# Kernel tuning notes

Hardware: AMD Instinct MI355X
Metric: run time of the kernel (lower is better)

Reference implementation:

```python
import jax, jax.numpy as jnp
import numpy as np

TAU = 0.07
HARD_RATIO = 0.3
N_T = 8192
N_S = 8192
F_DIM = 128
P_DIM = 128
BN_EPS = 1e-5
GRID_B, GRID_Z, GRID_Y, GRID_X = 2, 64, 128, 128


def _project(x, w1, b1, w2, b2, gamma, beta):
    # Linear -> ReLU -> Linear -> BatchNorm1d (training-mode batch stats) -> L2 normalize
    h = jax.nn.relu(x @ w1 + b1)
    h = h @ w2 + b2
    mu = h.mean(axis=0)
    var = h.var(axis=0)  # biased, matching torch BN normalization
    h = (h - mu) * jax.lax.rsqrt(var + BN_EPS) * gamma + beta
    return h / jnp.linalg.norm(h, axis=1, keepdims=True)


def _coord_key(c):
    # unique int key per (b,z,y,x) cell; fits easily in int32 for this grid
    return ((c[:, 0] * GRID_Z + c[:, 1]) * GRID_Y + c[:, 2]) * GRID_X + c[:, 3]


def setup_inputs() -> dict:
    rng = np.random.default_rng(0)
    total = GRID_B * GRID_Z * GRID_Y * GRID_X
    perm = rng.permutation(total)
    t_lin = perm[:N_T]  # unique teacher voxel cells
    n_overlap = N_S // 2  # half the student voxels coincide with teacher voxels
    s_lin = np.concatenate([t_lin[:n_overlap], perm[N_T:N_T + (N_S - n_overlap)]])
    s_lin = rng.permutation(s_lin)

    def lin2coord(l):
        x = l % GRID_X; l = l // GRID_X
        y = l % GRID_Y; l = l // GRID_Y
        z = l % GRID_Z; b = l // GRID_Z
        return np.stack([b, z, y, x], axis=1).astype(np.int32)

    key = jax.random.key(0)
    ks = jax.random.split(key, 8)

    def lin_w(k, fan_in, fan_out):
        return jax.random.normal(k, (fan_in, fan_out), jnp.float32) / np.float32(np.sqrt(fan_in))

    return {
        'teacher_features': jax.random.normal(ks[0], (N_T, F_DIM), jnp.float32),
        'student_features': jax.random.normal(ks[1], (N_S, F_DIM), jnp.float32),
        't_w1': lin_w(ks[2], F_DIM, F_DIM), 't_b1': jnp.zeros((F_DIM,), jnp.float32),
        't_w2': lin_w(ks[3], F_DIM, P_DIM), 't_b2': jnp.zeros((P_DIM,), jnp.float32),
        't_gamma': jnp.ones((P_DIM,), jnp.float32), 't_beta': jnp.zeros((P_DIM,), jnp.float32),
        's_w1': lin_w(ks[4], F_DIM, F_DIM), 's_b1': jnp.zeros((F_DIM,), jnp.float32),
        's_w2': lin_w(ks[5], F_DIM, P_DIM), 's_b2': jnp.zeros((P_DIM,), jnp.float32),
        's_gamma': jnp.ones((P_DIM,), jnp.float32), 's_beta': jnp.zeros((P_DIM,), jnp.float32),
        'teacher_coords': jnp.asarray(lin2coord(t_lin)),
        'student_coords': jnp.asarray(lin2coord(s_lin)),
    }


def reference(teacher_features, student_features,
              t_w1, t_b1, t_w2, t_b2, t_gamma, t_beta,
              s_w1, s_b1, s_w2, s_b2, s_gamma, s_beta,
              teacher_coords, student_coords):
    t_proj = _project(teacher_features, t_w1, t_b1, t_w2, t_b2, t_gamma, t_beta)  # [N_t, P]
    s_proj = _project(student_features, s_w1, s_b1, s_w2, s_b2, s_gamma, s_beta)  # [N_s, P]

    # hash-based positive matching (teacher coords are unique cells)
    tk = _coord_key(teacher_coords)  # [N_t]
    sk = _coord_key(student_coords)  # [N_s]
    eq = sk[:, None] == tk[None, :]  # [N_s, N_t] bool
    matched = eq.any(axis=1)         # [N_s]
    t_idx = jnp.argmax(eq, axis=1)   # matching teacher index (garbage where unmatched, masked below)

    pos_sim = jnp.sum(s_proj * t_proj[t_idx], axis=1) / TAU  # [N_s]
    neg_sim = (s_proj @ t_proj.T) / TAU                       # [N_s, N_t] full teacher pool

    # hard negative mining: top-k most similar negatives per student
    k = max(1, int(N_T * HARD_RATIO))
    hard_neg, _ = jax.lax.top_k(neg_sim, k)                   # [N_s, k]

    all_sims = jnp.concatenate([pos_sim[:, None], hard_neg], axis=1)  # [N_s, 1+k]
    per_pair = -jax.nn.log_softmax(all_sims, axis=1)[:, 0]

    m = matched.astype(per_pair.dtype)
    loss = jnp.sum(per_pair * m) / jnp.maximum(jnp.sum(m), 1.0)
    return loss
```

## Files before the change

kernel.cpp:

```cpp
#include <hip/hip_runtime.h>
#include <hip/hip_bf16.h>

#define NT 8192
#define NS 8192
#define FD 128
#define PD 128
#define KTOP 2457
#define TAUINV 14.285714285714286f
#define NBIN 512
#define HSIZE 65536
#define HMASK 65535
#define CAND_MAX 1024
#define NMC 4096

typedef __attribute__((ext_vector_type(8))) short s16x8;
typedef __attribute__((ext_vector_type(4))) float f32x4;

__device__ __forceinline__ float bf2f(unsigned short u) {
  return __uint_as_float(((unsigned)u) << 16);
}
__device__ __forceinline__ unsigned short f2bf(float x) {
  unsigned u = __float_as_uint(x);
  return (unsigned short)((u + 0x7FFF + ((u >> 16) & 1)) >> 16);
}

__global__ __launch_bounds__(256) void init_ws(float* stats, int* hkey, int* nmatch)
{
  int i = blockIdx.x * 256 + threadIdx.x;
  if (i < 512) stats[i] = 0.f;
  if (i < HSIZE) hkey[i] = -1;
  if (i == 0) *nmatch = 0;
}

__global__ __launch_bounds__(256) void proj_mlp2(
    const float* __restrict__ Xt, const float* __restrict__ Xs2,
    const float* __restrict__ tW1, const float* __restrict__ tB1,
    const float* __restrict__ tW2, const float* __restrict__ tB2,
    const float* __restrict__ sW1, const float* __restrict__ sB1,
    const float* __restrict__ sW2, const float* __restrict__ sB2,
    float* __restrict__ Ht, float* __restrict__ Hs2, float* __restrict__ stats)
{
  int f = blockIdx.y;
  const float* X  = f ? Xs2 : Xt;
  const float* W1 = f ? sW1 : tW1;
  const float* B1 = f ? sB1 : tB1;
  const float* W2 = f ? sW2 : tW2;
  const float* B2 = f ? sB2 : tB2;
  float* H        = f ? Hs2 : Ht;
  float* colsum   = stats + f * 256;
  float* colsq    = colsum + 128;

  __shared__ __align__(16) float Xs[32][128];
  __shared__ __align__(16) float H1s[32][128];
  __shared__ float cs[128], cq[128];
  int tid = threadIdx.x;
  int r0 = blockIdx.x * 32;
  for (int i = tid; i < 32 * 32; i += 256) {
    int r = i >> 5, q = i & 31;
    ((float4*)Xs[r])[q] = ((const float4*)(X + (size_t)(r0 + r) * FD))[q];
  }
  if (tid < 128) { cs[tid] = 0.f; cq[tid] = 0.f; }
  __syncthreads();

  int c  = (tid & 63) * 2;
  int rg = (tid >> 6) * 8;
  float a0[8], a1[8];
  #pragma unroll
  for (int r = 0; r < 8; ++r) { a0[r] = 0.f; a1[r] = 0.f; }
  for (int k = 0; k < FD; ++k) {
    float2 w = *(const float2*)(W1 + k * FD + c);
    #pragma unroll
    for (int r = 0; r < 8; ++r) {
      float x = Xs[rg + r][k];
      a0[r] = fmaf(x, w.x, a0[r]);
      a1[r] = fmaf(x, w.y, a1[r]);
    }
  }
  float2 b = *(const float2*)(B1 + c);
  #pragma unroll
  for (int r = 0; r < 8; ++r) {
    H1s[rg + r][c]     = fmaxf(a0[r] + b.x, 0.f);
    H1s[rg + r][c + 1] = fmaxf(a1[r] + b.y, 0.f);
  }
  __syncthreads();

  #pragma unroll
  for (int r = 0; r < 8; ++r) { a0[r] = 0.f; a1[r] = 0.f; }
  for (int k = 0; k < FD; ++k) {
    float2 w = *(const float2*)(W2 + k * PD + c);
    #pragma unroll
    for (int r = 0; r < 8; ++r) {
      float x = H1s[rg + r][k];
      a0[r] = fmaf(x, w.x, a0[r]);
      a1[r] = fmaf(x, w.y, a1[r]);
    }
  }
  b = *(const float2*)(B2 + c);
  float s0 = 0.f, s1 = 0.f, q0 = 0.f, q1 = 0.f;
  #pragma unroll
  for (int r = 0; r < 8; ++r) {
    float h0 = a0[r] + b.x, h1 = a1[r] + b.y;
    *(float2*)(H + (size_t)(r0 + rg + r) * PD + c) = make_float2(h0, h1);
    s0 += h0; s1 += h1; q0 += h0 * h0; q1 += h1 * h1;
  }
  atomicAdd(&cs[c], s0);     atomicAdd(&cs[c + 1], s1);
  atomicAdd(&cq[c], q0);     atomicAdd(&cq[c + 1], q1);
  __syncthreads();
  if (tid < 128) { atomicAdd(&colsum[tid], cs[tid]); atomicAdd(&colsq[tid], cq[tid]); }
}

__global__ __launch_bounds__(256) void bn_l2_2(
    const float* __restrict__ Ht, const float* __restrict__ Hs2,
    const float* __restrict__ stats,
    const float* __restrict__ t_gamma, const float* __restrict__ t_beta,
    const float* __restrict__ s_gamma, const float* __restrict__ s_beta,
    unsigned short* __restrict__ Th, unsigned short* __restrict__ Tl,
    unsigned short* __restrict__ ShC, unsigned short* __restrict__ SlC,
    const int* __restrict__ minv)
{
  int f = blockIdx.y;
  const float* H = f ? Hs2 : Ht;
  const float* colsum = stats + f * 256;
  const float* colsq  = colsum + 128;
  const float* gamma  = f ? s_gamma : t_gamma;
  const float* beta   = f ? s_beta : t_beta;
  unsigned short* Oh  = f ? ShC : Th;
  unsigned short* Ol  = f ? SlC : Tl;
  const float invN = 1.f / (float)NT;

  __shared__ float part[2][2];
  int half = threadIdx.x >> 7;
  int c    = threadIdx.x & 127;
  int wih  = (threadIdx.x >> 6) & 1;
  int row  = blockIdx.x * 2 + half;
  float mu  = colsum[c] * invN;
  float var = colsq[c] * invN - mu * mu;
  float inv = rsqrtf(var + 1e-5f);
  float y = (H[(size_t)row * PD + c] - mu) * inv * gamma[c] + beta[c];
  float sq = y * y;
  #pragma unroll
  for (int off = 32; off >= 1; off >>= 1) sq += __shfl_xor(sq, off, 64);
  if ((threadIdx.x & 63) == 0) part[half][wih] = sq;
  __syncthreads();
  float norm = sqrtf(part[half][0] + part[half][1]);
  float r = y / norm;
  int orow = f ? minv[row] : row;
  if (orow >= 0) {
    unsigned ub = __float_as_uint(r);
    float fhi = __uint_as_float(ub & 0xFFFF0000u);
    float lo  = r - fhi;
    Oh[(size_t)orow * PD + c] = (unsigned short)(ub >> 16);
    Ol[(size_t)orow * PD + c] = (unsigned short)(__float_as_uint(lo) >> 16);
  }
}

__device__ __forceinline__ int coord_key(int4 c) {
  return ((c.x * 64 + c.y) * 128 + c.z) * 128 + c.w;
}

__global__ __launch_bounds__(256) void hash_insert(
    const int* __restrict__ coords, int* __restrict__ hkey, int* __restrict__ hval)
{
  int t = blockIdx.x * 256 + threadIdx.x;
  if (t >= NT) return;
  int key = coord_key(((const int4*)coords)[t]);
  unsigned slot = (((unsigned)key * 2654435761u) >> 16) & HMASK;
  while (true) {
    int old = atomicCAS(&hkey[slot], -1, key);
    if (old == -1) { hval[slot] = t; break; }
    slot = (slot + 1) & HMASK;
  }
}

__global__ __launch_bounds__(256) void hash_lookup(
    const int* __restrict__ coords, const int* __restrict__ hkey,
    const int* __restrict__ hval, int* __restrict__ minv,
    int* __restrict__ mt, int* __restrict__ nmatch)
{
  int s = blockIdx.x * 256 + threadIdx.x;
  if (s >= NS) return;
  int key = coord_key(((const int4*)coords)[s]);
  unsigned slot = (((unsigned)key * 2654435761u) >> 16) & HMASK;
  int res = -1;
  while (true) {
    int k = hkey[slot];
    if (k == key) { res = hval[slot]; break; }
    if (k == -1) break;
    slot = (slot + 1) & HMASK;
  }
  int cslot = -1;
  if (res >= 0) { cslot = atomicAdd(nmatch, 1); mt[cslot] = res; }
  minv[s] = cslot;
}

__global__ __launch_bounds__(256) void pos_exact(
    const unsigned short* __restrict__ ShC, const unsigned short* __restrict__ SlC,
    const unsigned short* __restrict__ Th, const unsigned short* __restrict__ Tl,
    const int* __restrict__ mt, const int* __restrict__ nmatch,
    float* __restrict__ posb)
{
  int lane = threadIdx.x & 63, wid = threadIdx.x >> 6;
  int slot = blockIdx.x * 4 + wid;
  if (slot >= *nmatch) return;
  int t = mt[slot];
  const unsigned short* ah = ShC + (size_t)slot * FD;
  const unsigned short* al = SlC + (size_t)slot * FD;
  const unsigned short* bh = Th + (size_t)t * FD;
  const unsigned short* bl = Tl + (size_t)t * FD;
  float sum = 0.f;
  #pragma unroll
  for (int j = 0; j < 2; ++j) {
    int k = lane * 2 + j;
    float av = bf2f(ah[k]) + bf2f(al[k]);
    float bv = bf2f(bh[k]) + bf2f(bl[k]);
    sum = fmaf(av, bv, sum);
  }
  #pragma unroll
  for (int off = 32; off >= 1; off >>= 1) sum += __shfl_xor(sum, off, 64);
  if (lane == 0) posb[slot] = sum * TAUINV;
}

__device__ __forceinline__ void gload16(const void* g, void* l) {
  __builtin_amdgcn_global_load_lds(
      (const __attribute__((address_space(1))) unsigned int*)g,
      (__attribute__((address_space(3))) unsigned int*)l, 16, 0, 0);
}

__global__ __launch_bounds__(256) void gemm_bf16x2(
    const unsigned short* __restrict__ ShC, const unsigned short* __restrict__ SlC,
    const unsigned short* __restrict__ Th, const unsigned short* __restrict__ Tl,
    unsigned short* __restrict__ Pb, const int* __restrict__ nmatch)
{
  int ay = blockIdx.x, bx = blockIdx.y;
  if (ay * 128 >= *nmatch) return;

  __shared__ unsigned short lds[32768];
  int tid = threadIdx.x, lane = tid & 63, wid = tid >> 6;

  const unsigned short* gB[2] = { Th + (size_t)bx * 128 * FD,
                                  Tl + (size_t)bx * 128 * FD };
  #pragma unroll
  for (int comp = 0; comp < 2; ++comp) {
    const char* g = (const char*)gB[comp];
    char* lb = (char*)lds + comp * 32768;
    #pragma unroll
    for (int it = 0; it < 8; ++it) {
      int chunk0 = it * 256 + wid * 64;
      int d = (chunk0 + lane) * 16;
      int src = d ^ (((d >> 8) & 7) << 4);
      gload16(g + src, lb + chunk0 * 16);
    }
  }

  int wr = wid >> 1, wc = wid & 1;
  const unsigned short* gA_h = ShC + (size_t)(ay * 128) * FD;
  const unsigned short* gA_l = SlC + (size_t)(ay * 128) * FD;
  int rA[4];
  #pragma unroll
  for (int m = 0; m < 4; ++m) rA[m] = wr * 64 + m * 16 + (lane & 15);
  int cA0 = (lane >> 4) * 8;

  s16x8 nah[4], nal[4];
  #pragma unroll
  for (int m = 0; m < 4; ++m) {
    nah[m] = *(const s16x8*)(gA_h + (size_t)rA[m] * FD + cA0);
    nal[m] = *(const s16x8*)(gA_l + (size_t)rA[m] * FD + cA0);
  }
  __syncthreads();

  f32x4 acc[4][4] = {};
  #pragma unroll
  for (int kk = 0; kk < 4; ++kk) {
    s16x8 ah[4], al[4];
    #pragma unroll
    for (int m = 0; m < 4; ++m) { ah[m] = nah[m]; al[m] = nal[m]; }
    if (kk < 3) {
      int cA = (kk + 1) * 32 + cA0;
      #pragma unroll
      for (int m = 0; m < 4; ++m) {
        nah[m] = *(const s16x8*)(gA_h + (size_t)rA[m] * FD + cA);
        nal[m] = *(const s16x8*)(gA_l + (size_t)rA[m] * FD + cA);
      }
    }
    int cB = kk * 32 + cA0;
    s16x8 bh[4], bl[4];
    #pragma unroll
    for (int n = 0; n < 4; ++n) {
      int r = wc * 64 + n * 16 + (lane & 15);
      int byt = r * 256 + ((cB * 2) ^ ((r & 7) << 4));
      bh[n] = *(const s16x8*)((const char*)lds + byt);
      bl[n] = *(const s16x8*)((const char*)lds + 32768 + byt);
    }
    #pragma unroll
    for (int m = 0; m < 4; ++m)
      #pragma unroll
      for (int n = 0; n < 4; ++n) {
        acc[m][n] = __builtin_amdgcn_mfma_f32_16x16x32_bf16(ah[m], bh[n], acc[m][n], 0, 0, 0);
        acc[m][n] = __builtin_amdgcn_mfma_f32_16x16x32_bf16(ah[m], bl[n], acc[m][n], 0, 0, 0);
        acc[m][n] = __builtin_amdgcn_mfma_f32_16x16x32_bf16(al[m], bh[n], acc[m][n], 0, 0, 0);
      }
  }

  #pragma unroll
  for (int m = 0; m < 4; ++m)
    #pragma unroll
    for (int n = 0; n < 4; ++n) {
      int pc = bx * 128 + wc * 64 + n * 16 + (lane & 15);
      int pr0 = ay * 128 + wr * 64 + m * 16 + (lane >> 4) * 4;
      #pragma unroll
      for (int reg = 0; reg < 4; ++reg)
        Pb[(size_t)(pr0 + reg) * NT + pc] = f2bf(acc[m][n][reg] * TAUINV);
    }
}

__global__ __launch_bounds__(256) void select_lse(
    const unsigned short* __restrict__ Pb, const float* __restrict__ posb,
    const int* __restrict__ nmatch, float* __restrict__ perrow)
{
  int slot = blockIdx.x;
  if (slot >= *nmatch) return;

  __shared__ unsigned hist4[4 * NBIN];
  __shared__ unsigned cnt[NBIN];
  __shared__ float cand[CAND_MAX];
  __shared__ float red[4];
  __shared__ int redi[4];
  __shared__ float sh_lo[3], sh_scale[3];
  __shared__ int sh_bin[3];
  __shared__ int sh_B, sh_jrem, sh_cntB;
  __shared__ unsigned sh_cc;
  __shared__ float sh_M;
  __shared__ float sh_theta;

  int tid = threadIdx.x, lane = tid & 63, wid = tid >> 6;
  const unsigned short* p = Pb + (size_t)slot * NT;

  float rr[32];
  float mx = -1e30f;
  #pragma unroll
  for (int q = 0; q < 4; ++q) {
    s16x8 v = ((const s16x8*)p)[tid + 256 * q];
    #pragma unroll
    for (int j = 0; j < 8; ++j) {
      float f = bf2f((unsigned short)v[j]);
      rr[q * 8 + j] = f;
      mx = fmaxf(mx, f);
    }
  }
  #pragma unroll
  for (int off = 32; off >= 1; off >>= 1) mx = fmaxf(mx, __shfl_xor(mx, off, 64));
  if (lane == 0) red[wid] = mx;
  __syncthreads();
  if (tid == 0) sh_M = fmaxf(fmaxf(red[0], red[1]), fmaxf(red[2], red[3]));

  int kneed = KTOP;
  float lo = -14.6f, hi = 14.6f;
  int nlev = 0, jrem = 0, cntB = 0;
  for (int level = 0; level < 3; ++level) {
    float scale = (float)NBIN / (hi - lo);
    for (int i = tid; i < 4 * NBIN; i += 256) hist4[i] = 0;
    __syncthreads();
    unsigned* wh = hist4 + wid * NBIN;
    #pragma unroll
    for (int j = 0; j < 32; ++j) {
      float v = rr[j];
      bool act = true;
      for (int l = 0; l < nlev; ++l) {
        int bb = (int)((v - sh_lo[l]) * sh_scale[l]);
        bb = bb < 0 ? 0 : (bb > NBIN - 1 ? NBIN - 1 : bb);
        act = act && (bb == sh_bin[l]);
      }
      if (act) {
        int bb = (int)((v - lo) * scale);
        bb = bb < 0 ? 0 : (bb > NBIN - 1 ? NBIN - 1 : bb);
        atomicAdd(&wh[bb], 1u);
      }
    }
    __syncthreads();
    for (int i = tid; i < NBIN; i += 256)
      cnt[i] = hist4[i] + hist4[NBIN + i] + hist4[2 * NBIN + i] + hist4[3 * NBIN + i];
    __syncthreads();
    for (int off = 1; off < NBIN; off <<= 1) {
      unsigned c0 = (tid + off < NBIN) ? cnt[tid + off] : 0u;
      unsigned c1 = (tid + 256 + off < NBIN) ? cnt[tid + 256 + off] : 0u;
      __syncthreads();
      cnt[tid] += c0;
      cnt[tid + 256] += c1;
      __syncthreads();
    }
    #pragma unroll
    for (int u = 0; u < 2; ++u) {
      int i = tid + u * 256;
      unsigned si = cnt[i];
      unsigned sn = (i < NBIN - 1) ? cnt[i + 1] : 0u;
      if (si >= (unsigned)kneed && sn < (unsigned)kneed) {
        sh_B = i;
        sh_jrem = kneed - (int)sn;
        sh_cntB = (int)(si - sn);
      }
    }
    __syncthreads();
    int B = sh_B; jrem = sh_jrem; cntB = sh_cntB;
    if (tid == 0) { sh_lo[level] = lo; sh_scale[level] = scale; sh_bin[level] = B; }
    nlev = level + 1;
    if (cntB <= CAND_MAX) break;
    float wdt = (hi - lo) * (1.0f / NBIN);
    lo = lo + (float)B * wdt;
    hi = lo + wdt;
    kneed = jrem;
    __syncthreads();
  }

  if (tid == 0) sh_cc = 0;
  __syncthreads();
  #pragma unroll
  for (int j = 0; j < 32; ++j) {
    float v = rr[j];
    bool act = true;
    for (int l = 0; l < nlev; ++l) {
      int bb = (int)((v - sh_lo[l]) * sh_scale[l]);
      bb = bb < 0 ? 0 : (bb > NBIN - 1 ? NBIN - 1 : bb);
      act = act && (bb == sh_bin[l]);
    }
    if (act) {
      unsigned idx = atomicAdd(&sh_cc, 1u);
      if (idx < CAND_MAX) cand[idx] = v;
    }
  }
  __syncthreads();
  int c = (int)sh_cc; if (c > CAND_MAX) c = CAND_MAX;

  float thl = -1e30f;
  for (int i = tid; i < c; i += 256) {
    float v = cand[i];
    int gt = 0, eq = 0;
    for (int m = 0; m < c; ++m) {
      float u = cand[m];
      gt += (u > v) ? 1 : 0;
      eq += (u == v) ? 1 : 0;
    }
    if (gt < jrem && jrem <= gt + eq) thl = v;
  }
  #pragma unroll
  for (int off = 32; off >= 1; off >>= 1) thl = fmaxf(thl, __shfl_xor(thl, off, 64));
  if (lane == 0) red[wid] = thl;
  __syncthreads();
  if (tid == 0) sh_theta = fmaxf(fmaxf(red[0], red[1]), fmaxf(red[2], red[3]));
  __syncthreads();
  float theta = sh_theta;
  float pos = posb[slot];
  float Mp = fmaxf(sh_M, pos);

  float esum = 0.f; int g = 0;
  #pragma unroll
  for (int j = 0; j < 32; ++j) {
    float v = rr[j];
    if (v > theta) { esum += __expf(v - Mp); g++; }
  }
  #pragma unroll
  for (int off = 32; off >= 1; off >>= 1) {
    esum += __shfl_xor(esum, off, 64);
    g    += __shfl_xor(g, off, 64);
  }
  if (lane == 0) { red[wid] = esum; redi[wid] = g; }
  __syncthreads();
  if (tid == 0) {
    float E = red[0] + red[1] + red[2] + red[3];
    int   G = redi[0] + redi[1] + redi[2] + redi[3];
    float S = E + (float)(KTOP - G) * __expf(theta - Mp) + __expf(pos - Mp);
    perrow[slot] = logf(S) + Mp - pos;
  }
}

__global__ __launch_bounds__(256) void finalize(
    const float* __restrict__ perrow, const int* __restrict__ nmatch,
    float* __restrict__ out)
{
  __shared__ float ssum[4];
  int nm = *nmatch;
  float s = 0.f;
  for (int i = threadIdx.x; i < nm; i += 256) s += perrow[i];
  #pragma unroll
  for (int off = 32; off >= 1; off >>= 1) s += __shfl_xor(s, off, 64);
  int lane = threadIdx.x & 63, wid = threadIdx.x >> 6;
  if (lane == 0) ssum[wid] = s;
  __syncthreads();
  if (threadIdx.x == 0) {
    float S = ssum[0] + ssum[1] + ssum[2] + ssum[3];
    out[0] = S / fmaxf((float)nm, 1.f);
  }
}

extern "C" void kernel_launch(void* const* d_in, const int* in_sizes, int n_in,
                              void* d_out, int out_size, void* d_ws, size_t ws_size,
                              hipStream_t stream)
{
  const float* t_feat  = (const float*)d_in[0];
  const float* s_feat  = (const float*)d_in[1];
  const float* t_w1    = (const float*)d_in[2];
  const float* t_b1    = (const float*)d_in[3];
  const float* t_w2    = (const float*)d_in[4];
  const float* t_b2    = (const float*)d_in[5];
  const float* t_gamma = (const float*)d_in[6];
  const float* t_beta  = (const float*)d_in[7];
  const float* s_w1    = (const float*)d_in[8];
  const float* s_b1    = (const float*)d_in[9];
  const float* s_w2    = (const float*)d_in[10];
  const float* s_b2    = (const float*)d_in[11];
  const float* s_gamma = (const float*)d_in[12];
  const float* s_beta  = (const float*)d_in[13];
  const int*   t_coord = (const int*)d_in[14];
  const int*   s_coord = (const int*)d_in[15];

  char* w = (char*)d_ws;
  unsigned short* Th  = (unsigned short*)(w + 0x000000);
  unsigned short* Tl  = (unsigned short*)(w + 0x200000);
  unsigned short* ShC = (unsigned short*)(w + 0x400000);
  unsigned short* SlC = (unsigned short*)(w + 0x600000);
  float* stats  = (float*)(w + 0x800000);
  int*   hkey   = (int*)(w + 0x800800);
  int*   hval   = (int*)(w + 0x840800);
  int*   nmatch = (int*)(w + 0x880800);
  int*   mt     = (int*)(w + 0x880900);
  int*   minv   = (int*)(w + 0x888900);
  float* perrow = (float*)(w + 0x890900);
  float* posb   = (float*)(w + 0x898900);
  float* Ht     = (float*)(w + 0x8B0000);
  float* Hs     = (float*)(w + 0xCB0000);
  unsigned short* Pb = (unsigned short*)(w + 0x8B0000);

  init_ws<<<HSIZE / 256, 256, 0, stream>>>(stats, hkey, nmatch);
  hash_insert<<<NT / 256, 256, 0, stream>>>(t_coord, hkey, hval);
  hash_lookup<<<NS / 256, 256, 0, stream>>>(s_coord, hkey, hval, minv, mt, nmatch);

  {
    dim3 g(NT / 32, 2);
    proj_mlp2<<<g, 256, 0, stream>>>(t_feat, s_feat,
                                     t_w1, t_b1, t_w2, t_b2,
                                     s_w1, s_b1, s_w2, s_b2,
                                     Ht, Hs, stats);
  }
  {
    dim3 g(NT / 2, 2);
    bn_l2_2<<<g, 256, 0, stream>>>(Ht, Hs, stats, t_gamma, t_beta,
                                   s_gamma, s_beta, Th, Tl, ShC, SlC, minv);
  }
  pos_exact<<<NMC / 4, 256, 0, stream>>>(ShC, SlC, Th, Tl, mt, nmatch, posb);

  {
    dim3 g(NMC / 128, NT / 128);
    gemm_bf16x2<<<g, 256, 0, stream>>>(ShC, SlC, Th, Tl, Pb, nmatch);
  }
  select_lse<<<NMC, 256, 0, stream>>>(Pb, posb, nmatch, perrow);
  finalize<<<1, 256, 0, stream>>>(perrow, nmatch, (float*)d_out);
}
```

Before: 255.6 us.

## Use exact 2-pass radix select on bf16 keys and fuse pos/finalize into select

```diff
diff --git a/kernel.cpp b/kernel.cpp
--- a/kernel.cpp
+++ b/kernel.cpp
@@ -7,10 +7,8 @@
 #define PD 128
 #define KTOP 2457
 #define TAUINV 14.285714285714286f
-#define NBIN 512
 #define HSIZE 65536
 #define HMASK 65535
-#define CAND_MAX 1024
 #define NMC 4096
 
 typedef __attribute__((ext_vector_type(8))) short s16x8;
@@ -23,13 +21,22 @@
   unsigned u = __float_as_uint(x);
   return (unsigned short)((u + 0x7FFF + ((u >> 16) & 1)) >> 16);
 }
-
-__global__ __launch_bounds__(256) void init_ws(float* stats, int* hkey, int* nmatch)
+__device__ __forceinline__ unsigned bf2key(unsigned short u) {
+  return (u & 0x8000u) ? (unsigned)(u ^ 0xFFFFu) : (unsigned)(u ^ 0x8000u);
+}
+__device__ __forceinline__ float key2f(unsigned key) {
+  unsigned u = (key & 0x8000u) ? (key ^ 0x8000u) : (key ^ 0xFFFFu);
+  return __uint_as_float((u & 0xFFFFu) << 16);
+}
+
+__global__ __launch_bounds__(256) void init_ws(float* stats, int* hkey,
+                                               int* nmatch, float* dsum,
+                                               unsigned* dcnt)
 {
   int i = blockIdx.x * 256 + threadIdx.x;
   if (i < 512) stats[i] = 0.f;
   if (i < HSIZE) hkey[i] = -1;
-  if (i == 0) *nmatch = 0;
+  if (i == 0) { *nmatch = 0; *dsum = 0.f; *dcnt = 0u; }
 }
 
 __global__ __launch_bounds__(256) void proj_mlp2(
@@ -193,33 +200,6 @@
   minv[s] = cslot;
 }
 
-__global__ __launch_bounds__(256) void pos_exact(
-    const unsigned short* __restrict__ ShC, const unsigned short* __restrict__ SlC,
-    const unsigned short* __restrict__ Th, const unsigned short* __restrict__ Tl,
-    const int* __restrict__ mt, const int* __restrict__ nmatch,
-    float* __restrict__ posb)
-{
-  int lane = threadIdx.x & 63, wid = threadIdx.x >> 6;
-  int slot = blockIdx.x * 4 + wid;
-  if (slot >= *nmatch) return;
-  int t = mt[slot];
-  const unsigned short* ah = ShC + (size_t)slot * FD;
-  const unsigned short* al = SlC + (size_t)slot * FD;
-  const unsigned short* bh = Th + (size_t)t * FD;
-  const unsigned short* bl = Tl + (size_t)t * FD;
-  float sum = 0.f;
-  #pragma unroll
-  for (int j = 0; j < 2; ++j) {
-    int k = lane * 2 + j;
-    float av = bf2f(ah[k]) + bf2f(al[k]);
-    float bv = bf2f(bh[k]) + bf2f(bl[k]);
-    sum = fmaf(av, bv, sum);
-  }
-  #pragma unroll
-  for (int off = 32; off >= 1; off >>= 1) sum += __shfl_xor(sum, off, 64);
-  if (lane == 0) posb[slot] = sum * TAUINV;
-}
-
 __device__ __forceinline__ void gload16(const void* g, void* l) {
   __builtin_amdgcn_global_load_lds(
       (const __attribute__((address_space(1))) unsigned int*)g,
@@ -314,180 +294,151 @@
 }
 
 __global__ __launch_bounds__(256) void select_lse(
-    const unsigned short* __restrict__ Pb, const float* __restrict__ posb,
-    const int* __restrict__ nmatch, float* __restrict__ perrow)
-{
+    const unsigned short* __restrict__ Pb,
+    const unsigned short* __restrict__ ShC, const unsigned short* __restrict__ SlC,
+    const unsigned short* __restrict__ Th, const unsigned short* __restrict__ Tl,
+    const int* __restrict__ mt, const int* __restrict__ nmatch,
+    float* __restrict__ dsum, unsigned* __restrict__ dcnt,
+    float* __restrict__ out)
+{
+  __shared__ unsigned hist4[4 * 256];
+  __shared__ unsigned wsum[4];
+  __shared__ float redF[4];
+  __shared__ unsigned redU[4];
+  __shared__ int redI[4];
+  __shared__ unsigned sh_Mk;
+  __shared__ float sh_pos;
+  __shared__ int sh_B1, sh_B2;
+  __shared__ unsigned sh_j1;
+
+  int tid = threadIdx.x, lane = tid & 63, wid = tid >> 6;
   int slot = blockIdx.x;
-  if (slot >= *nmatch) return;
-
-  __shared__ unsigned hist4[4 * NBIN];
-  __shared__ unsigned cnt[NBIN];
-  __shared__ float cand[CAND_MAX];
-  __shared__ float red[4];
-  __shared__ int redi[4];
-  __shared__ float sh_lo[3], sh_scale[3];
-  __shared__ int sh_bin[3];
-  __shared__ int sh_B, sh_jrem, sh_cntB;
-  __shared__ unsigned sh_cc;
-  __shared__ float sh_M;
-  __shared__ float sh_theta;
-
-  int tid = threadIdx.x, lane = tid & 63, wid = tid >> 6;
-  const unsigned short* p = Pb + (size_t)slot * NT;
-
-  float rr[32];
-  float mx = -1e30f;
-  #pragma unroll
-  for (int q = 0; q < 4; ++q) {
-    s16x8 v = ((const s16x8*)p)[tid + 256 * q];
-    #pragma unroll
-    for (int j = 0; j < 8; ++j) {
-      float f = bf2f((unsigned short)v[j]);
-      rr[q * 8 + j] = f;
-      mx = fmaxf(mx, f);
-    }
-  }
-  #pragma unroll
-  for (int off = 32; off >= 1; off >>= 1) mx = fmaxf(mx, __shfl_xor(mx, off, 64));
-  if (lane == 0) red[wid] = mx;
-  __syncthreads();
-  if (tid == 0) sh_M = fmaxf(fmaxf(red[0], red[1]), fmaxf(red[2], red[3]));
-
-  int kneed = KTOP;
-  float lo = -14.6f, hi = 14.6f;
-  int nlev = 0, jrem = 0, cntB = 0;
-  for (int level = 0; level < 3; ++level) {
-    float scale = (float)NBIN / (hi - lo);
-    for (int i = tid; i < 4 * NBIN; i += 256) hist4[i] = 0;
-    __syncthreads();
-    unsigned* wh = hist4 + wid * NBIN;
+  int nm = *nmatch;
+  bool active = slot < nm;
+
+  if (active) {
+    const unsigned short* p = Pb + (size_t)slot * NT;
+
+    if (wid == 0) {
+      int t = mt[slot];
+      int k0 = lane * 2;
+      float a0 = bf2f(ShC[(size_t)slot * FD + k0])     + bf2f(SlC[(size_t)slot * FD + k0]);
+      float a1 = bf2f(ShC[(size_t)slot * FD + k0 + 1]) + bf2f(SlC[(size_t)slot * FD + k0 + 1]);
+      float b0 = bf2f(Th[(size_t)t * FD + k0])         + bf2f(Tl[(size_t)t * FD + k0]);
+      float b1 = bf2f(Th[(size_t)t * FD + k0 + 1])     + bf2f(Tl[(size_t)t * FD + k0 + 1]);
+      float sum = fmaf(a1, b1, a0 * b0);
+      #pragma unroll
+      for (int off = 32; off >= 1; off >>= 1) sum += __shfl_xor(sum, off, 64);
+      if (lane == 0) sh_pos = sum * TAUINV;
+    }
+
+    unsigned kk[32];
+    unsigned kmax = 0;
+    #pragma unroll
+    for (int q = 0; q < 4; ++q) {
+      s16x8 v = ((const s16x8*)p)[tid + 256 * q];
+      #pragma unroll
+      for (int j = 0; j < 8; ++j) {
+        unsigned key = bf2key((unsigned short)v[j]);
+        kk[q * 8 + j] = key;
+        kmax = key > kmax ? key : kmax;
+      }
+    }
+    #pragma unroll
+    for (int off = 32; off >= 1; off >>= 1) {
+      unsigned o = __shfl_xor(kmax, off, 64);
+      kmax = o > kmax ? o : kmax;
+    }
+    if (lane == 0) redU[wid] = kmax;
+    __syncthreads();
+    if (tid == 0) {
+      unsigned m0 = redU[0] > redU[1] ? redU[0] : redU[1];
+      unsigned m1 = redU[2] > redU[3] ? redU[2] : redU[3];
+      sh_Mk = m0 > m1 ? m0 : m1;
+    }
+
+    hist4[tid] = 0; hist4[tid + 256] = 0; hist4[tid + 512] = 0; hist4[tid + 768] = 0;
+    __syncthreads();
+    unsigned* wh = hist4 + (wid << 8);
+    #pragma unroll
+    for (int j = 0; j < 32; ++j) atomicAdd(&wh[kk[j] >> 8], 1u);
+    __syncthreads();
+    unsigned c0 = hist4[tid] + hist4[tid + 256] + hist4[tid + 512] + hist4[tid + 768];
+    unsigned s = c0;
+    #pragma unroll
+    for (int off = 1; off <= 32; off <<= 1) {
+      unsigned t2 = __shfl_down(s, off, 64);
+      if (lane + off < 64) s += t2;
+    }
+    if (lane == 0) wsum[wid] = s;
+    __syncthreads();
+    unsigned add = 0;
+    for (int w2 = wid + 1; w2 < 4; ++w2) add += wsum[w2];
+    unsigned si = s + add, sn = si - c0;
+    if (si >= (unsigned)KTOP && sn < (unsigned)KTOP) {
+      sh_B1 = tid;
+      sh_j1 = (unsigned)KTOP - sn;
+    }
+    __syncthreads();
+    int B1 = sh_B1;
+    unsigned j1 = sh_j1;
+
+    hist4[tid] = 0; hist4[tid + 256] = 0; hist4[tid + 512] = 0; hist4[tid + 768] = 0;
+    __syncthreads();
+    #pragma unroll
+    for (int j = 0; j < 32; ++j)
+      if ((int)(kk[j] >> 8) == B1) atomicAdd(&wh[kk[j] & 255], 1u);
+    __syncthreads();
+    c0 = hist4[tid] + hist4[tid + 256] + hist4[tid + 512] + hist4[tid + 768];
+    s = c0;
+    #pragma unroll
+    for (int off = 1; off <= 32; off <<= 1) {
+      unsigned t2 = __shfl_down(s, off, 64);
+      if (lane + off < 64) s += t2;
+    }
+    if (lane == 0) wsum[wid] = s;
+    __syncthreads();
+    add = 0;
+    for (int w2 = wid + 1; w2 < 4; ++w2) add += wsum[w2];
+    si = s + add; sn = si - c0;
+    if (si >= j1 && sn < j1) sh_B2 = tid;
+    __syncthreads();
+
+    unsigned kth = ((unsigned)sh_B1 << 8) | (unsigned)sh_B2;
+    float theta = key2f(kth);
+    float M = key2f(sh_Mk);
+    float pos = sh_pos;
+    float Mp = fmaxf(M, pos);
+
+    float esum = 0.f; int g = 0;
     #pragma unroll
     for (int j = 0; j < 32; ++j) {
-      float v = rr[j];
-      bool act = true;
-      for (int l = 0; l < nlev; ++l) {
-        int bb = (int)((v - sh_lo[l]) * sh_scale[l]);
-        bb = bb < 0 ? 0 : (bb > NBIN - 1 ? NBIN - 1 : bb);
-        act = act && (bb == sh_bin[l]);
-      }
-      if (act) {
-        int bb = (int)((v - lo) * scale);
-        bb = bb < 0 ? 0 : (bb > NBIN - 1 ? NBIN - 1 : bb);
-        atomicAdd(&wh[bb], 1u);
-      }
-    }
-    __syncthreads();
-    for (int i = tid; i < NBIN; i += 256)
-      cnt[i] = hist4[i] + hist4[NBIN + i] + hist4[2 * NBIN + i] + hist4[3 * NBIN + i];
-    __syncthreads();
-    for (int off = 1; off < NBIN; off <<= 1) {
-      unsigned c0 = (tid + off < NBIN) ? cnt[tid + off] : 0u;
-      unsigned c1 = (tid + 256 + off < NBIN) ? cnt[tid + 256 + off] : 0u;
-      __syncthreads();
-      cnt[tid] += c0;
-      cnt[tid + 256] += c1;
-      __syncthreads();
-    }
-    #pragma unroll
-    for (int u = 0; u < 2; ++u) {
-      int i = tid + u * 256;
-      unsigned si = cnt[i];
-      unsigned sn = (i < NBIN - 1) ? cnt[i + 1] : 0u;
-      if (si >= (unsigned)kneed && sn < (unsigned)kneed) {
-        sh_B = i;
-        sh_jrem = kneed - (int)sn;
-        sh_cntB = (int)(si - sn);
-      }
-    }
-    __syncthreads();
-    int B = sh_B; jrem = sh_jrem; cntB = sh_cntB;
-    if (tid == 0) { sh_lo[level] = lo; sh_scale[level] = scale; sh_bin[level] = B; }
-    nlev = level + 1;
-    if (cntB <= CAND_MAX) break;
-    float wdt = (hi - lo) * (1.0f / NBIN);
-    lo = lo + (float)B * wdt;
-    hi = lo + wdt;
-    kneed = jrem;
-    __syncthreads();
-  }
-
-  if (tid == 0) sh_cc = 0;
-  __syncthreads();
-  #pragma unroll
-  for (int j = 0; j < 32; ++j) {
-    float v = rr[j];
-    bool act = true;
-    for (int l = 0; l < nlev; ++l) {
-      int bb = (int)((v - sh_lo[l]) * sh_scale[l]);
-      bb = bb < 0 ? 0 : (bb > NBIN - 1 ? NBIN - 1 : bb);
-      act = act && (bb == sh_bin[l]);
-    }
-    if (act) {
-      unsigned idx = atomicAdd(&sh_cc, 1u);
-      if (idx < CAND_MAX) cand[idx] = v;
-    }
-  }
-  __syncthreads();
-  int c = (int)sh_cc; if (c > CAND_MAX) c = CAND_MAX;
-
-  float thl = -1e30f;
-  for (int i = tid; i < c; i += 256) {
-    float v = cand[i];
-    int gt = 0, eq = 0;
-    for (int m = 0; m < c; ++m) {
-      float u = cand[m];
-      gt += (u > v) ? 1 : 0;
-      eq += (u == v) ? 1 : 0;
-    }
-    if (gt < jrem && jrem <= gt + eq) thl = v;
-  }
-  #pragma unroll
-  for (int off = 32; off >= 1; off >>= 1) thl = fmaxf(thl, __shfl_xor(thl, off, 64));
-  if (lane == 0) red[wid] = thl;
-  __syncthreads();
-  if (tid == 0) sh_theta = fmaxf(fmaxf(red[0], red[1]), fmaxf(red[2], red[3]));
-  __syncthreads();
-  float theta = sh_theta;
-  float pos = posb[slot];
-  float Mp = fmaxf(sh_M, pos);
-
-  float esum = 0.f; int g = 0;
-  #pragma unroll
-  for (int j = 0; j < 32; ++j) {
-    float v = rr[j];
-    if (v > theta) { esum += __expf(v - Mp); g++; }
-  }
-  #pragma unroll
-  for (int off = 32; off >= 1; off >>= 1) {
-    esum += __shfl_xor(esum, off, 64);
-    g    += __shfl_xor(g, off, 64);
-  }
-  if (lane == 0) { red[wid] = esum; redi[wid] = g; }
-  __syncthreads();
+      float v = key2f(kk[j]);
+      if (v > theta) { esum += __expf(v - Mp); g++; }
+    }
+    #pragma unroll
+    for (int off = 32; off >= 1; off >>= 1) {
+      esum += __shfl_xor(esum, off, 64);
+      g    += __shfl_xor(g, off, 64);
+    }
+    if (lane == 0) { redF[wid] = esum; redI[wid] = g; }
+    __syncthreads();
+    if (tid == 0) {
+      float E = redF[0] + redF[1] + redF[2] + redF[3];
+      int   G = redI[0] + redI[1] + redI[2] + redI[3];
+      float S = E + (float)(KTOP - G) * __expf(theta - Mp) + __expf(pos - Mp);
+      atomicAdd(dsum, logf(S) + Mp - pos);
+    }
+  }
+
+  __threadfence();
   if (tid == 0) {
-    float E = red[0] + red[1] + red[2] + red[3];
-    int   G = redi[0] + redi[1] + redi[2] + redi[3];
-    float S = E + (float)(KTOP - G) * __expf(theta - Mp) + __expf(pos - Mp);
-    perrow[slot] = logf(S) + Mp - pos;
-  }
-}
-
-__global__ __launch_bounds__(256) void finalize(
-    const float* __restrict__ perrow, const int* __restrict__ nmatch,
-    float* __restrict__ out)
-{
-  __shared__ float ssum[4];
-  int nm = *nmatch;
-  float s = 0.f;
-  for (int i = threadIdx.x; i < nm; i += 256) s += perrow[i];
-  #pragma unroll
-  for (int off = 32; off >= 1; off >>= 1) s += __shfl_xor(s, off, 64);
-  int lane = threadIdx.x & 63, wid = threadIdx.x >> 6;
-  if (lane == 0) ssum[wid] = s;
-  __syncthreads();
-  if (threadIdx.x == 0) {
-    float S = ssum[0] + ssum[1] + ssum[2] + ssum[3];
-    out[0] = S / fmaxf((float)nm, 1.f);
+    unsigned old = atomicAdd(dcnt, 1u);
+    if (old == (unsigned)gridDim.x - 1u) {
+      __threadfence();
+      float S = *(volatile float*)dsum;
+      out[0] = S / fmaxf((float)nm, 1.f);
+    }
   }
 }
 
@@ -523,13 +474,13 @@
   int*   nmatch = (int*)(w + 0x880800);
   int*   mt     = (int*)(w + 0x880900);
   int*   minv   = (int*)(w + 0x888900);
-  float* perrow = (float*)(w + 0x890900);
-  float* posb   = (float*)(w + 0x898900);
+  float* dsum   = (float*)(w + 0x890900);
+  unsigned* dcnt = (unsigned*)(w + 0x890908);
   float* Ht     = (float*)(w + 0x8B0000);
   float* Hs     = (float*)(w + 0xCB0000);
   unsigned short* Pb = (unsigned short*)(w + 0x8B0000);
 
-  init_ws<<<HSIZE / 256, 256, 0, stream>>>(stats, hkey, nmatch);
+  init_ws<<<HSIZE / 256, 256, 0, stream>>>(stats, hkey, nmatch, dsum, dcnt);
   hash_insert<<<NT / 256, 256, 0, stream>>>(t_coord, hkey, hval);
   hash_lookup<<<NS / 256, 256, 0, stream>>>(s_coord, hkey, hval, minv, mt, nmatch);
 
@@ -545,12 +496,10 @@
     bn_l2_2<<<g, 256, 0, stream>>>(Ht, Hs, stats, t_gamma, t_beta,
                                    s_gamma, s_beta, Th, Tl, ShC, SlC, minv);
   }
-  pos_exact<<<NMC / 4, 256, 0, stream>>>(ShC, SlC, Th, Tl, mt, nmatch, posb);
-
   {
     dim3 g(NMC / 128, NT / 128);
     gemm_bf16x2<<<g, 256, 0, stream>>>(ShC, SlC, Th, Tl, Pb, nmatch);
   }
-  select_lse<<<NMC, 256, 0, stream>>>(Pb, posb, nmatch, perrow);
-  finalize<<<1, 256, 0, stream>>>(perrow, nmatch, (float*)d_out);
-}
+  select_lse<<<NMC, 256, 0, stream>>>(Pb, ShC, SlC, Th, Tl, mt, nmatch,
+                                      dsum, dcnt, (float*)d_out);
+}
```

Result: slower. 465.0 us (+81.9%).
